# Optimization experiments

Measured on AMD Instinct MI355X. Metric: run time of the kernel, lower is better.

The kernel has to match this reference:

```python
import jax, jax.numpy as jnp
import numpy as np

EPS = 1e-7

def _logmap0(x):
    # Poincare ball (c=1) log map at the origin: artanh(||x||) * x/||x||
    n = jnp.linalg.norm(x, axis=-1, keepdims=True)
    n = jnp.clip(n, EPS, 1.0 - EPS)
    return jnp.arctanh(n) * x / n

def _expmap0(v):
    # Poincare ball (c=1) exp map at the origin: tanh(||v||) * v/||v||
    n = jnp.maximum(jnp.linalg.norm(v, axis=-1, keepdims=True), EPS)
    return jnp.tanh(n) * v / n

def setup_inputs() -> dict:
    N, E, DIN, DOUT = 100000, 1000000, 512, 512
    key = jax.random.key(0)
    k1, k2, k3, k4, k5, k6 = jax.random.split(key, 6)
    g = jax.random.normal(k1, (N, DIN), jnp.float32)
    # points strictly inside the unit ball (valid Poincare coordinates)
    r = 0.9 * jax.random.uniform(k2, (N, 1), jnp.float32)
    x = g / jnp.maximum(jnp.linalg.norm(g, axis=-1, keepdims=True), 1e-6) * r
    src = jax.random.randint(k3, (E,), 0, N)
    dst = jax.random.randint(k4, (E,), 0, N)
    W = jax.random.normal(k5, (DOUT, DIN), jnp.float32) / np.sqrt(DIN).astype(np.float32)
    b = jax.random.normal(k6, (DOUT,), jnp.float32) * 0.01
    return {"x": x, "src": src, "dst": dst, "W": W, "b": b}

def reference(x, src, dst, W, b):
    N = x.shape[0]
    tangent = _logmap0(x)                      # [N, din]
    h = tangent @ W.T + b                      # [N, dout] (nn.Linear)
    # DGL update_all(copy_u, mean): mean over incoming edges per dst node;
    # zero-in-degree nodes get 0 (DGL convention).
    sums = jax.ops.segment_sum(h[src], dst, num_segments=N)          # [N, dout]
    deg = jax.ops.segment_sum(jnp.ones_like(dst, dtype=h.dtype), dst, num_segments=N)
    neigh = sums / jnp.maximum(deg, 1.0)[:, None]
    return _expmap0(neigh)
```

## Files before the change

### kernel.cpp

```cpp
#include <hip/hip_runtime.h>
#include <stdint.h>

#define DIN 512
#define DOUT 512

typedef short bf16x8 __attribute__((ext_vector_type(8)));
typedef float floatx4 __attribute__((ext_vector_type(4)));
typedef float f32x4 __attribute__((ext_vector_type(4)));

static __device__ __forceinline__ ushort f2bf(float f) {
  uint32_t u = __float_as_uint(f);
  u += 0x7FFFu + ((u >> 16) & 1u);
  return (ushort)(u >> 16);
}

static __device__ __forceinline__ void gload16(const ushort* g, ushort* l) {
  __builtin_amdgcn_global_load_lds(
      (const __attribute__((address_space(1))) unsigned int*)g,
      (__attribute__((address_space(3))) unsigned int*)l, 16, 0, 0);
}

__global__ __launch_bounds__(256) void fused1_kernel(
    const float* __restrict__ x, ushort* __restrict__ tanb,
    const float* __restrict__ W, ushort* __restrict__ Wbf,
    const int* __restrict__ dst, int* __restrict__ degi, int N, int E) {
  int bid = blockIdx.x;
  int degB = (E + 255) >> 8;
  if (bid < degB) {
    int e = bid * 256 + threadIdx.x;
    if (e < E) atomicAdd(&degi[dst[e]], 1);
    return;
  }
  bid -= degB;
  int logB = (N + 3) >> 2;
  if (bid < logB) {
    int row = bid * 4 + (threadIdx.x >> 6);
    if (row >= N) return;
    int lane = threadIdx.x & 63;
    const f32x4* xr = (const f32x4*)(x + (size_t)row * DIN);
    f32x4 v0 = __builtin_nontemporal_load(xr + lane * 2);
    f32x4 v1 = __builtin_nontemporal_load(xr + lane * 2 + 1);
    float ss = v0[0]*v0[0] + v0[1]*v0[1] + v0[2]*v0[2] + v0[3]*v0[3] +
               v1[0]*v1[0] + v1[1]*v1[1] + v1[2]*v1[2] + v1[3]*v1[3];
#pragma unroll
    for (int m = 32; m >= 1; m >>= 1) ss += __shfl_xor(ss, m, 64);
    float n = sqrtf(ss);
    float nc = fminf(fmaxf(n, 1e-7f), 1.0f - 1e-7f);
    float scale = atanhf(nc) / nc;
    union { ushort s[8]; uint4 v; } o;
    o.s[0] = f2bf(v0[0] * scale); o.s[1] = f2bf(v0[1] * scale);
    o.s[2] = f2bf(v0[2] * scale); o.s[3] = f2bf(v0[3] * scale);
    o.s[4] = f2bf(v1[0] * scale); o.s[5] = f2bf(v1[1] * scale);
    o.s[6] = f2bf(v1[2] * scale); o.s[7] = f2bf(v1[3] * scale);
    *(uint4*)(tanb + (size_t)row * DIN + lane * 8) = o.v;
    return;
  }
  bid -= logB;
  int i = bid * 1024 + threadIdx.x * 4;
  float4 w4 = *(const float4*)(W + i);
  ushort4 o4;
  o4.x = f2bf(w4.x); o4.y = f2bf(w4.y); o4.z = f2bf(w4.z); o4.w = f2bf(w4.w);
  *(ushort4*)(Wbf + i) = o4;
}

__global__ __launch_bounds__(256) void scan1_kernel(const int* __restrict__ degi,
                                                    int* __restrict__ offs,
                                                    int* __restrict__ bsum, int N) {
  __shared__ int s[256];
  int tx = threadIdx.x;
  int i = blockIdx.x * 256 + tx;
  int v = (i < N) ? degi[i] : 0;
  s[tx] = v;
  __syncthreads();
#pragma unroll
  for (int d = 1; d < 256; d <<= 1) {
    int t = (tx >= d) ? s[tx - d] : 0;
    __syncthreads();
    s[tx] += t;
    __syncthreads();
  }
  if (i < N) offs[i] = s[tx] - v;
  if (tx == 255) bsum[blockIdx.x] = s[255];
}

__global__ __launch_bounds__(1024) void scan2_kernel(int* __restrict__ bsum, int B) {
  __shared__ int s[1024];
  int tx = threadIdx.x;
  int v = (tx < B) ? bsum[tx] : 0;
  s[tx] = v;
  __syncthreads();
#pragma unroll
  for (int d = 1; d < 1024; d <<= 1) {
    int t = (tx >= d) ? s[tx - d] : 0;
    __syncthreads();
    s[tx] += t;
    __syncthreads();
  }
  if (tx < B) bsum[tx] = s[tx] - v;
}

__global__ __launch_bounds__(256) void scan3_kernel(int* __restrict__ offs,
                                                    const int* __restrict__ bsum,
                                                    int* __restrict__ cursor, int N) {
  int i = blockIdx.x * 256 + threadIdx.x;
  if (i < N) {
    int o = offs[i] + bsum[blockIdx.x];
    offs[i] = o;
    cursor[i] = o;
  }
}

__global__ __launch_bounds__(256) void gemmfill_kernel(
    const ushort* __restrict__ A, const ushort* __restrict__ Bw,
    const float* __restrict__ bias, ushort* __restrict__ Hb, int M,
    const int* __restrict__ src, const int* __restrict__ dst,
    int* __restrict__ cursor, int* __restrict__ adj, int E, int FB) {
  __shared__ __align__(16) ushort smem[16384];
  int bid = blockIdx.x;
  if (bid < FB) {
    int e = bid * 256 + threadIdx.x;
    if (e < E) {
      int pos = atomicAdd(&cursor[dst[e]], 1);
      adj[pos] = src[e];
    }
    return;
  }
  bid -= FB;
  int NB = (int)gridDim.x - FB;
  int q = NB >> 3, r = NB & 7;
  int xcd = bid & 7, off = bid >> 3;
  int w = (xcd < r) ? xcd * (q + 1) + off : r * (q + 1) + (xcd - r) * q + off;
  int n0 = (w & 3) * 128;
  int m0 = (w >> 2) * 128;

  ushort* As = smem;
  ushort* Bs = smem + 8192;
  int tid = threadIdx.x;
  int wave = tid >> 6, lane = tid & 63;
  int wm = (wave >> 1) * 64, wn = (wave & 1) * 64;
  int fr = lane & 15, fq = lane >> 4;
  int rsub = lane >> 3;
  int ksw = ((lane & 7) ^ rsub) * 8;

  floatx4 acc[4][4] = {};

  for (int k0 = 0; k0 < DIN; k0 += 64) {
#pragma unroll
    for (int i = 0; i < 4; i++) {
      int g = wave * 4 + i;
      int ra = g * 8 + rsub;
      int gm = m0 + ra; if (gm >= M) gm = M - 1;
      gload16(A + (size_t)gm * DIN + k0 + ksw, As + g * 512);
      gload16(Bw + (size_t)(n0 + ra) * DIN + k0 + ksw, Bs + g * 512);
    }
    __syncthreads();
#pragma unroll
    for (int kk = 0; kk < 2; kk++) {
      bf16x8 af[4], bg[4];
#pragma unroll
      for (int t = 0; t < 4; t++) {
        int ra = wm + t * 16 + fr;
        af[t] = *(const bf16x8*)(As + ra * 64 + (((kk * 4 + fq) ^ (ra & 7)) << 3));
        int rb = wn + t * 16 + fr;
        bg[t] = *(const bf16x8*)(Bs + rb * 64 + (((kk * 4 + fq) ^ (rb & 7)) << 3));
      }
#pragma unroll
      for (int mt = 0; mt < 4; mt++)
#pragma unroll
        for (int nt = 0; nt < 4; nt++)
          acc[mt][nt] = __builtin_amdgcn_mfma_f32_16x16x32_bf16(
              af[mt], bg[nt], acc[mt][nt], 0, 0, 0);
    }
    __syncthreads();
  }

  int rq = fq * 4;
#pragma unroll
  for (int nt = 0; nt < 4; nt++) {
    int col = wn + nt * 16 + fr;
    float bb = bias[n0 + col];
    int c16 = col >> 3;
#pragma unroll
    for (int mt = 0; mt < 4; mt++) {
#pragma unroll
      for (int rr = 0; rr < 4; rr++) {
        int row = wm + mt * 16 + rq + rr;
        smem[row * 128 + (((c16 ^ (row & 7)) << 3) | (col & 7))] =
            f2bf(acc[mt][nt][rr] + bb);
      }
    }
  }
  __syncthreads();
#pragma unroll
  for (int p = 0; p < 8; p++) {
    int idx = p * 256 + tid;
    int row = idx >> 4, cc = idx & 15;
    uint4 v = *(const uint4*)(smem + row * 128 + ((cc ^ (row & 7)) << 3));
    int gm = m0 + row;
    if (gm < M) *(uint4*)(Hb + (size_t)gm * DOUT + n0 + cc * 8) = v;
  }
}

static __device__ __forceinline__ void accum8(float* acc, uint4 v) {
  acc[0] += __uint_as_float(v.x << 16); acc[1] += __uint_as_float(v.x & 0xFFFF0000u);
  acc[2] += __uint_as_float(v.y << 16); acc[3] += __uint_as_float(v.y & 0xFFFF0000u);
  acc[4] += __uint_as_float(v.z << 16); acc[5] += __uint_as_float(v.z & 0xFFFF0000u);
  acc[6] += __uint_as_float(v.w << 16); acc[7] += __uint_as_float(v.w & 0xFFFF0000u);
}

__global__ __launch_bounds__(256) void aggregate_kernel(const ushort* __restrict__ hb,
                                                        const int* __restrict__ adj,
                                                        const int* __restrict__ offs,
                                                        const int* __restrict__ degi,
                                                        float* __restrict__ out, int N) {
  int row = blockIdx.x * 4 + (threadIdx.x >> 6);
  if (row >= N) return;
  int lane = threadIdx.x & 63;
  int dg = degi[row];
  int base = offs[row];
  float acc[8] = {0.f, 0.f, 0.f, 0.f, 0.f, 0.f, 0.f, 0.f};
  int j = 0;
  for (; j + 8 <= dg; j += 8) {
    int av = adj[base + j + (lane & 7)];
    uint4 v[8];
#pragma unroll
    for (int qq = 0; qq < 8; qq++) {
      int s = __builtin_amdgcn_readlane(av, qq);
      v[qq] = *(const uint4*)(hb + (size_t)s * DOUT + lane * 8);
    }
#pragma unroll
    for (int qq = 0; qq < 8; qq++) accum8(acc, v[qq]);
  }
  for (; j + 4 <= dg; j += 4) {
    int av = adj[base + j + (lane & 3)];
    uint4 v[4];
#pragma unroll
    for (int qq = 0; qq < 4; qq++) {
      int s = __builtin_amdgcn_readlane(av, qq);
      v[qq] = *(const uint4*)(hb + (size_t)s * DOUT + lane * 8);
    }
#pragma unroll
    for (int qq = 0; qq < 4; qq++) accum8(acc, v[qq]);
  }
  for (; j < dg; j++) {
    int s = __builtin_amdgcn_readfirstlane(adj[base + j]);
    uint4 a = *(const uint4*)(hb + (size_t)s * DOUT + lane * 8);
    accum8(acc, a);
  }
  float inv = 1.0f / fmaxf((float)dg, 1.0f);
  float ss = 0.f;
#pragma unroll
  for (int k = 0; k < 8; k++) ss += acc[k] * acc[k];
#pragma unroll
  for (int m = 32; m >= 1; m >>= 1) ss += __shfl_xor(ss, m, 64);
  float n = fmaxf(inv * sqrtf(ss), 1e-7f);
  float sc = tanhf(n) / n * inv;
  f32x4 o0 = {acc[0] * sc, acc[1] * sc, acc[2] * sc, acc[3] * sc};
  f32x4 o1 = {acc[4] * sc, acc[5] * sc, acc[6] * sc, acc[7] * sc};
  float* orow = out + (size_t)row * DOUT + lane * 8;
  __builtin_nontemporal_store(o0, (f32x4*)orow);
  __builtin_nontemporal_store(o1, (f32x4*)(orow + 4));
}

extern "C" void kernel_launch(void* const* d_in, const int* in_sizes, int n_in,
                              void* d_out, int out_size, void* d_ws, size_t ws_size,
                              hipStream_t stream) {
  const float* x = (const float*)d_in[0];
  const int* src = (const int*)d_in[1];
  const int* dst = (const int*)d_in[2];
  const float* W = (const float*)d_in[3];
  const float* b = (const float*)d_in[4];
  int N = in_sizes[0] / DIN;
  int E = in_sizes[1];
  float* out = (float*)d_out;

  char* ws = (char*)d_ws;
  size_t off = 0;
  ushort* Wbf = (ushort*)(ws + off); off += (size_t)DOUT * DIN * 2;
  ushort* tanb = (ushort*)(ws + off); off += (size_t)N * DIN * 2;
  ushort* hb = (ushort*)(ws + off); off += (size_t)N * DIN * 2;
  off = (off + 255) & ~(size_t)255;
  int* degi = (int*)(ws + off); off += (size_t)N * 4;
  off = (off + 255) & ~(size_t)255;
  int* offs = (int*)(ws + off); off += (size_t)N * 4;
  off = (off + 255) & ~(size_t)255;
  int* cursor = (int*)(ws + off); off += (size_t)N * 4;
  off = (off + 255) & ~(size_t)255;
  int* bsum = (int*)(ws + off); off += 1024 * 4;
  int* adj = (int*)(ws + off); off += (size_t)E * 4;

  hipMemsetAsync(degi, 0, (size_t)N * 4, stream);

  int degB = (E + 255) >> 8;
  int logB = (N + 3) >> 2;
  int wB = (DOUT * DIN) / 1024;
  fused1_kernel<<<degB + logB + wB, 256, 0, stream>>>(x, tanb, W, Wbf, dst, degi, N, E);

  int B1 = (N + 255) / 256;
  scan1_kernel<<<B1, 256, 0, stream>>>(degi, offs, bsum, N);
  scan2_kernel<<<1, 1024, 0, stream>>>(bsum, B1);
  scan3_kernel<<<B1, 256, 0, stream>>>(offs, bsum, cursor, N);

  int MB = (N + 127) >> 7;
  int FB = degB;
  gemmfill_kernel<<<FB + 4 * MB, 256, 0, stream>>>(tanb, Wbf, b, hb, N,
                                                   src, dst, cursor, adj, E, FB);

  aggregate_kernel<<<(N + 3) / 4, 256, 0, stream>>>(hb, adj, offs, degi, out, N);
}
```

Baseline: 653.9 us.

## Record per-edge rank during degree count and replace three-pass scan with single-block scan

The degree-counting atomic now stores its returned value as a per-edge rank (ushort), so the CSR fill writes adj[offs[dst]+rank] without a second atomic pass on a cursor array. The three scan kernels are merged into one 1024-thread block that serially sums about 100 degrees per thread, scans in shared memory, then writes the offsets. This cuts two kernel launches and the fill-phase atomics, at the cost of an extra E*2-byte rank array and a single-block scan with poorly coalesced per-thread strided reads. The ushort rank assumes no node has in-degree of 65536 or more.

```diff
diff --git a/kernel.cpp b/kernel.cpp
--- a/kernel.cpp
+++ b/kernel.cpp
@@ -23,12 +23,16 @@
 __global__ __launch_bounds__(256) void fused1_kernel(
     const float* __restrict__ x, ushort* __restrict__ tanb,
     const float* __restrict__ W, ushort* __restrict__ Wbf,
-    const int* __restrict__ dst, int* __restrict__ degi, int N, int E) {
+    const int* __restrict__ dst, int* __restrict__ degi,
+    ushort* __restrict__ rank, int N, int E) {
   int bid = blockIdx.x;
   int degB = (E + 255) >> 8;
   if (bid < degB) {
     int e = bid * 256 + threadIdx.x;
-    if (e < E) atomicAdd(&degi[dst[e]], 1);
+    if (e < E) {
+      int r = atomicAdd(&degi[dst[e]], 1);
+      rank[e] = (ushort)r;
+    }
     return;
   }
   bid -= degB;
@@ -63,31 +67,22 @@
   *(ushort4*)(Wbf + i) = o4;
 }
 
-__global__ __launch_bounds__(256) void scan1_kernel(const int* __restrict__ degi,
-                                                    int* __restrict__ offs,
-                                                    int* __restrict__ bsum, int N) {
-  __shared__ int s[256];
-  int tx = threadIdx.x;
-  int i = blockIdx.x * 256 + tx;
-  int v = (i < N) ? degi[i] : 0;
-  s[tx] = v;
-  __syncthreads();
-#pragma unroll
-  for (int d = 1; d < 256; d <<= 1) {
-    int t = (tx >= d) ? s[tx - d] : 0;
-    __syncthreads();
-    s[tx] += t;
-    __syncthreads();
-  }
-  if (i < N) offs[i] = s[tx] - v;
-  if (tx == 255) bsum[blockIdx.x] = s[255];
-}
-
-__global__ __launch_bounds__(1024) void scan2_kernel(int* __restrict__ bsum, int B) {
+__global__ __launch_bounds__(1024) void scanall_kernel(const int* __restrict__ degi,
+                                                       int* __restrict__ offs, int N) {
   __shared__ int s[1024];
   int tx = threadIdx.x;
-  int v = (tx < B) ? bsum[tx] : 0;
-  s[tx] = v;
+  int chunk = (N + 1023) >> 10;
+  chunk = (chunk + 3) & ~3;
+  int lo = tx * chunk;
+  int hi = lo + chunk; if (hi > N) hi = N;
+  int sum = 0;
+  int i = lo;
+  for (; i + 4 <= hi; i += 4) {
+    int4 v = *(const int4*)(degi + i);
+    sum += v.x + v.y + v.z + v.w;
+  }
+  for (; i < hi; i++) sum += degi[i];
+  s[tx] = sum;
   __syncthreads();
 #pragma unroll
   for (int d = 1; d < 1024; d <<= 1) {
@@ -96,17 +91,11 @@
     s[tx] += t;
     __syncthreads();
   }
-  if (tx < B) bsum[tx] = s[tx] - v;
-}
-
-__global__ __launch_bounds__(256) void scan3_kernel(int* __restrict__ offs,
-                                                    const int* __restrict__ bsum,
-                                                    int* __restrict__ cursor, int N) {
-  int i = blockIdx.x * 256 + threadIdx.x;
-  if (i < N) {
-    int o = offs[i] + bsum[blockIdx.x];
-    offs[i] = o;
-    cursor[i] = o;
+  int base = s[tx] - sum;
+  for (i = lo; i < hi; i++) {
+    int v = degi[i];
+    offs[i] = base;
+    base += v;
   }
 }
 
@@ -114,14 +103,15 @@
     const ushort* __restrict__ A, const ushort* __restrict__ Bw,
     const float* __restrict__ bias, ushort* __restrict__ Hb, int M,
     const int* __restrict__ src, const int* __restrict__ dst,
-    int* __restrict__ cursor, int* __restrict__ adj, int E, int FB) {
+    const int* __restrict__ offs, const ushort* __restrict__ rank,
+    int* __restrict__ adj, int E, int FB) {
   __shared__ __align__(16) ushort smem[16384];
   int bid = blockIdx.x;
   if (bid < FB) {
     int e = bid * 256 + threadIdx.x;
     if (e < E) {
-      int pos = atomicAdd(&cursor[dst[e]], 1);
-      adj[pos] = src[e];
+      int d = dst[e];
+      adj[offs[d] + (int)rank[e]] = src[e];
     }
     return;
   }
@@ -284,9 +274,8 @@
   off = (off + 255) & ~(size_t)255;
   int* offs = (int*)(ws + off); off += (size_t)N * 4;
   off = (off + 255) & ~(size_t)255;
-  int* cursor = (int*)(ws + off); off += (size_t)N * 4;
-  off = (off + 255) & ~(size_t)255;
-  int* bsum = (int*)(ws + off); off += 1024 * 4;
+  ushort* rank = (ushort*)(ws + off); off += (size_t)E * 2;
+  off = (off + 255) & ~(size_t)255;
   int* adj = (int*)(ws + off); off += (size_t)E * 4;
 
   hipMemsetAsync(degi, 0, (size_t)N * 4, stream);
@@ -294,17 +283,15 @@
   int degB = (E + 255) >> 8;
   int logB = (N + 3) >> 2;
   int wB = (DOUT * DIN) / 1024;
-  fused1_kernel<<<degB + logB + wB, 256, 0, stream>>>(x, tanb, W, Wbf, dst, degi, N, E);
-
-  int B1 = (N + 255) / 256;
-  scan1_kernel<<<B1, 256, 0, stream>>>(degi, offs, bsum, N);
-  scan2_kernel<<<1, 1024, 0, stream>>>(bsum, B1);
-  scan3_kernel<<<B1, 256, 0, stream>>>(offs, bsum, cursor, N);
+  fused1_kernel<<<degB + logB + wB, 256, 0, stream>>>(x, tanb, W, Wbf, dst, degi,
+                                                      rank, N, E);
+
+  scanall_kernel<<<1, 1024, 0, stream>>>(degi, offs, N);
 
   int MB = (N + 127) >> 7;
   int FB = degB;
   gemmfill_kernel<<<FB + 4 * MB, 256, 0, stream>>>(tanb, Wbf, b, hb, N,
-                                                   src, dst, cursor, adj, E, FB);
+                                                   src, dst, offs, rank, adj, E, FB);
 
   aggregate_kernel<<<(N + 3) / 4, 256, 0, stream>>>(hb, adj, offs, degi, out, N);
 }
```

Result: slower. 743.3 us (+13.7%).

## Replace global-atomic CSR build with two-level bucketed counting sort

Applied to the files above, without the earlier changes.

Builds the dst-sorted adjacency with a bucketed counting sort instead of global atomics. Per-block shared-memory histograms over 128-node buckets are scanned globally, edges are scattered into bucket-contiguous packed (src,dst-low) words, and the per-bucket local sort runs inside the GEMM launch. This removes the memset and the million global atomics on degree and cursor arrays, and improves locality of the adj writes. In exchange it adds a scatter kernel, an extra E-sized buffer, and bounds the packed src to 25 bits and NB to 1024.

```diff
diff --git a/kernel.cpp b/kernel.cpp
--- a/kernel.cpp
+++ b/kernel.cpp
@@ -3,6 +3,8 @@
 
 #define DIN 512
 #define DOUT 512
+#define HB 256
+#define BKT_SH 7
 
 typedef short bf16x8 __attribute__((ext_vector_type(8)));
 typedef float floatx4 __attribute__((ext_vector_type(4)));
@@ -23,20 +25,29 @@
 __global__ __launch_bounds__(256) void fused1_kernel(
     const float* __restrict__ x, ushort* __restrict__ tanb,
     const float* __restrict__ W, ushort* __restrict__ Wbf,
-    const int* __restrict__ dst, int* __restrict__ degi, int N, int E) {
+    const int* __restrict__ dst, int* __restrict__ ghist, int N, int E, int NB) {
+  __shared__ int hist[1024];
   int bid = blockIdx.x;
-  int degB = (E + 255) >> 8;
-  if (bid < degB) {
-    int e = bid * 256 + threadIdx.x;
-    if (e < E) atomicAdd(&degi[dst[e]], 1);
+  int tx = threadIdx.x;
+  if (bid < HB) {
+    for (int i = tx; i < NB; i += 256) hist[i] = 0;
+    __syncthreads();
+    int EPB = (E + HB - 1) / HB;
+    int e0 = bid * EPB;
+    int e1 = e0 + EPB; if (e1 > E) e1 = E;
+    for (int e = e0 + tx; e < e1; e += 256)
+      atomicAdd(&hist[dst[e] >> BKT_SH], 1);
+    __syncthreads();
+    for (int b = tx; b < NB; b += 256)
+      ghist[b * HB + bid] = hist[b];
     return;
   }
-  bid -= degB;
+  bid -= HB;
   int logB = (N + 3) >> 2;
   if (bid < logB) {
-    int row = bid * 4 + (threadIdx.x >> 6);
+    int row = bid * 4 + (tx >> 6);
     if (row >= N) return;
-    int lane = threadIdx.x & 63;
+    int lane = tx & 63;
     const f32x4* xr = (const f32x4*)(x + (size_t)row * DIN);
     f32x4 v0 = __builtin_nontemporal_load(xr + lane * 2);
     f32x4 v1 = __builtin_nontemporal_load(xr + lane * 2 + 1);
@@ -56,20 +67,20 @@
     return;
   }
   bid -= logB;
-  int i = bid * 1024 + threadIdx.x * 4;
+  int i = bid * 1024 + tx * 4;
   float4 w4 = *(const float4*)(W + i);
   ushort4 o4;
   o4.x = f2bf(w4.x); o4.y = f2bf(w4.y); o4.z = f2bf(w4.z); o4.w = f2bf(w4.w);
   *(ushort4*)(Wbf + i) = o4;
 }
 
-__global__ __launch_bounds__(256) void scan1_kernel(const int* __restrict__ degi,
-                                                    int* __restrict__ offs,
-                                                    int* __restrict__ bsum, int N) {
+__global__ __launch_bounds__(256) void scan1_kernel(const int* __restrict__ in,
+                                                    int* __restrict__ outp,
+                                                    int* __restrict__ bsum, int L) {
   __shared__ int s[256];
   int tx = threadIdx.x;
   int i = blockIdx.x * 256 + tx;
-  int v = (i < N) ? degi[i] : 0;
+  int v = (i < L) ? in[i] : 0;
   s[tx] = v;
   __syncthreads();
 #pragma unroll
@@ -79,7 +90,7 @@
     s[tx] += t;
     __syncthreads();
   }
-  if (i < N) offs[i] = s[tx] - v;
+  if (i < L) outp[i] = s[tx] - v;
   if (tx == 255) bsum[blockIdx.x] = s[255];
 }
 
@@ -99,35 +110,78 @@
   if (tx < B) bsum[tx] = s[tx] - v;
 }
 
-__global__ __launch_bounds__(256) void scan3_kernel(int* __restrict__ offs,
-                                                    const int* __restrict__ bsum,
-                                                    int* __restrict__ cursor, int N) {
+__global__ __launch_bounds__(256) void scan3_kernel(int* __restrict__ outp,
+                                                    const int* __restrict__ bsum, int L) {
   int i = blockIdx.x * 256 + threadIdx.x;
-  if (i < N) {
-    int o = offs[i] + bsum[blockIdx.x];
-    offs[i] = o;
-    cursor[i] = o;
+  if (i < L) outp[i] += bsum[blockIdx.x];
+}
+
+__global__ __launch_bounds__(256) void cscatter_kernel(
+    const int* __restrict__ src, const int* __restrict__ dst,
+    const int* __restrict__ gscan, uint32_t* __restrict__ cs, int E, int NB) {
+  __shared__ int lcur[1024];
+  int j = blockIdx.x, tx = threadIdx.x;
+  for (int b = tx; b < NB; b += 256) lcur[b] = gscan[b * HB + j];
+  __syncthreads();
+  int EPB = (E + HB - 1) / HB;
+  int e0 = j * EPB;
+  int e1 = e0 + EPB; if (e1 > E) e1 = E;
+  for (int e = e0 + tx; e < e1; e += 256) {
+    int d = dst[e];
+    int p = atomicAdd(&lcur[d >> BKT_SH], 1);
+    cs[p] = ((uint32_t)src[e] << BKT_SH) | (uint32_t)(d & ((1 << BKT_SH) - 1));
   }
 }
 
 __global__ __launch_bounds__(256) void gemmfill_kernel(
     const ushort* __restrict__ A, const ushort* __restrict__ Bw,
     const float* __restrict__ bias, ushort* __restrict__ Hb, int M,
-    const int* __restrict__ src, const int* __restrict__ dst,
-    int* __restrict__ cursor, int* __restrict__ adj, int E, int FB) {
+    const int* __restrict__ gscan, const uint32_t* __restrict__ cs,
+    int* __restrict__ adj, int* __restrict__ offs, int E, int NB, int FB) {
   __shared__ __align__(16) ushort smem[16384];
   int bid = blockIdx.x;
+  int tid = threadIdx.x;
   if (bid < FB) {
-    int e = bid * 256 + threadIdx.x;
-    if (e < E) {
-      int pos = atomicAdd(&cursor[dst[e]], 1);
-      adj[pos] = src[e];
+    int b = bid;
+    int S = gscan[b * HB];
+    int T = (b + 1 < NB) ? gscan[(b + 1) * HB] : E;
+    int base = b << BKT_SH;
+    int* sdeg = (int*)smem;
+    int* scur = sdeg + 128;
+    int* sscn = scur + 128;
+    if (tid < 128) sdeg[tid] = 0;
+    __syncthreads();
+    for (int e = S + tid; e < T; e += 256)
+      atomicAdd(&sdeg[cs[e] & 127], 1);
+    __syncthreads();
+    if (tid < 128) sscn[tid] = sdeg[tid];
+    __syncthreads();
+#pragma unroll
+    for (int d = 1; d < 128; d <<= 1) {
+      int t = (tid >= d && tid < 128) ? sscn[tid - d] : 0;
+      __syncthreads();
+      if (tid < 128) sscn[tid] += t;
+      __syncthreads();
+    }
+    if (tid < 128) {
+      int excl = sscn[tid] - sdeg[tid];
+      scur[tid] = excl;
+      int node = base + tid;
+      int Nn = NB << BKT_SH;  (void)Nn;
+      if (node < M) offs[node] = S + excl;
+    }
+    if (tid == 0 && b == NB - 1) offs[M] = E;
+    __syncthreads();
+    for (int e = S + tid; e < T; e += 256) {
+      uint32_t v = cs[e];
+      int p = atomicAdd(&scur[v & 127], 1);
+      adj[S + p] = (int)(v >> BKT_SH);
     }
     return;
   }
   bid -= FB;
-  int NB = (int)gridDim.x - FB;
-  int q = NB >> 3, r = NB & 7;
+  int TB = (int)gridDim.x - FB;
+  int q = TB >> 3, r = TB & 7;
   int xcd = bid & 7, off = bid >> 3;
   int w = (xcd < r) ? xcd * (q + 1) + off : r * (q + 1) + (xcd - r) * q + off;
   int n0 = (w & 3) * 128;
@@ -135,7 +189,6 @@
 
   ushort* As = smem;
   ushort* Bs = smem + 8192;
-  int tid = threadIdx.x;
   int wave = tid >> 6, lane = tid & 63;
   int wm = (wave >> 1) * 64, wn = (wave & 1) * 64;
   int fr = lane & 15, fq = lane >> 4;
@@ -211,13 +264,12 @@
 __global__ __launch_bounds__(256) void aggregate_kernel(const ushort* __restrict__ hb,
                                                         const int* __restrict__ adj,
                                                         const int* __restrict__ offs,
-                                                        const int* __restrict__ degi,
                                                         float* __restrict__ out, int N) {
   int row = blockIdx.x * 4 + (threadIdx.x >> 6);
   if (row >= N) return;
   int lane = threadIdx.x & 63;
-  int dg = degi[row];
   int base = offs[row];
+  int dg = offs[row + 1] - base;
   float acc[8] = {0.f, 0.f, 0.f, 0.f, 0.f, 0.f, 0.f, 0.f};
   int j = 0;
   for (; j + 8 <= dg; j += 8) {
@@ -274,37 +326,42 @@
   int E = in_sizes[1];
   float* out = (float*)d_out;
 
+  int NB = (N + 127) >> BKT_SH;
+  int L = NB * HB;
+
   char* ws = (char*)d_ws;
   size_t off = 0;
   ushort* Wbf = (ushort*)(ws + off); off += (size_t)DOUT * DIN * 2;
   ushort* tanb = (ushort*)(ws + off); off += (size_t)N * DIN * 2;
   ushort* hb = (ushort*)(ws + off); off += (size_t)N * DIN * 2;
   off = (off + 255) & ~(size_t)255;
-  int* degi = (int*)(ws + off); off += (size_t)N * 4;
-  off = (off + 255) & ~(size_t)255;
-  int* offs = (int*)(ws + off); off += (size_t)N * 4;
-  off = (off + 255) & ~(size_t)255;
-  int* cursor = (int*)(ws + off); off += (size_t)N * 4;
+  int* offs = (int*)(ws + off); off += (size_t)(N + 1) * 4;
+  off = (off + 255) & ~(size_t)255;
+  int* ghist = (int*)(ws + off); off += (size_t)L * 4;
+  off = (off + 255) & ~(size_t)255;
+  int* gscan = (int*)(ws + off); off += (size_t)L * 4;
   off = (off + 255) & ~(size_t)255;
   int* bsum = (int*)(ws + off); off += 1024 * 4;
+  off = (off + 255) & ~(size_t)255;
+  uint32_t* cs = (uint32_t*)(ws + off); off += (size_t)E * 4;
+  off = (off + 255) & ~(size_t)255;
   int* adj = (int*)(ws + off); off += (size_t)E * 4;
 
-  hipMemsetAsync(degi, 0, (size_t)N * 4, stream);
-
-  int degB = (E + 255) >> 8;
   int logB = (N + 3) >> 2;
   int wB = (DOUT * DIN) / 1024;
-  fused1_kernel<<<degB + logB + wB, 256, 0, stream>>>(x, tanb, W, Wbf, dst, degi, N, E);
-
-  int B1 = (N + 255) / 256;
-  scan1_kernel<<<B1, 256, 0, stream>>>(degi, offs, bsum, N);
-  scan2_kernel<<<1, 1024, 0, stream>>>(bsum, B1);
-  scan3_kernel<<<B1, 256, 0, stream>>>(offs, bsum, cursor, N);
+  fused1_kernel<<<HB + logB + wB, 256, 0, stream>>>(x, tanb, W, Wbf, dst, ghist,
+                                                    N, E, NB);
+
+  scan1_kernel<<<NB, 256, 0, stream>>>(ghist, gscan, bsum, L);
+  scan2_kernel<<<1, 1024, 0, stream>>>(bsum, NB);
+  scan3_kernel<<<NB, 256, 0, stream>>>(gscan, bsum, L);
+
+  cscatter_kernel<<<HB, 256, 0, stream>>>(src, dst, gscan, cs, E, NB);
 
   int MB = (N + 127) >> 7;
-  int FB = degB;
+  int FB = NB;
   gemmfill_kernel<<<FB + 4 * MB, 256, 0, stream>>>(tanb, Wbf, b, hb, N,
-                                                   src, dst, cursor, adj, E, FB);
-
-  aggregate_kernel<<<(N + 3) / 4, 256, 0, stream>>>(hb, adj, offs, degi, out, N);
-}
+                                                   gscan, cs, adj, offs, E, NB, FB);
+
+  aggregate_kernel<<<(N + 3) / 4, 256, 0, stream>>>(hb, adj, offs, out, N);
+}
```

After: 590.5 us. -9.7%, faster.
